# Optimization experiments

Hardware: AMD Instinct MI355X
Metric: run time of the kernel (lower is better)

Reference implementation:

```python
import jax, jax.numpy as jnp
import numpy as np

N = 250000   # number of occupied voxels (sparse points)
C = 64       # channels
G = 256      # voxel grid extent per axis
K = 3        # conv kernel size -> 27 offsets


def _build_neighbor_map():
    """Unique random voxel coords in a G^3 grid; nbr[i,o] = index of point at
    coords[i] + offset_o, or -1 if that voxel is unoccupied (torchsparse kernel map)."""
    rng = np.random.default_rng(0)
    keys = np.unique(rng.integers(0, G ** 3, size=2 * N, dtype=np.int64))[:N]  # sorted unique linearized coords
    x = keys // (G * G)
    y = (keys // G) % G
    z = keys % G
    nbr = np.full((N, K ** 3), -1, dtype=np.int32)
    o = 0
    for dx in (-1, 0, 1):
        for dy in (-1, 0, 1):
            for dz in (-1, 0, 1):
                cx, cy, cz = x + dx, y + dy, z + dz
                valid = (cx >= 0) & (cx < G) & (cy >= 0) & (cy < G) & (cz >= 0) & (cz < G)
                q = cx * (G * G) + cy * G + cz
                pos = np.searchsorted(keys, q).clip(0, N - 1)
                found = valid & (keys[pos] == q)
                nbr[:, o] = np.where(found, pos, -1).astype(np.int32)
                o += 1
    return nbr


def setup_inputs() -> dict:
    key = jax.random.key(0)
    ks = jax.random.split(key, 6)
    s = 0.05
    return {
        "feats": jax.random.normal(ks[0], (N, C), dtype=jnp.float32),
        "w00": jax.random.normal(ks[1], (K ** 3, C, C // 2), dtype=jnp.float32) * s,   # conv0_0: k=3
        "w01": jax.random.normal(ks[2], (K ** 3, C // 2, C // 2), dtype=jnp.float32) * s,  # conv0_1: k=3
        "w10": jax.random.normal(ks[3], (C, C // 2), dtype=jnp.float32) * s,           # conv1_0: 1x1
        "w11": jax.random.normal(ks[4], (K ** 3, C // 2, C // 2), dtype=jnp.float32) * s,  # conv1_1: k=3
        "w12": jax.random.normal(ks[5], (C // 2, C // 2), dtype=jnp.float32) * s,       # conv1_2: 1x1
        "nbr": jnp.asarray(_build_neighbor_map()),
    }


def _sparse_conv3(x, W, nbr):
    """Stride-1 sparse 3D conv: out[i] = sum_o W[o]^T x[nbr[i,o]], skipping absent voxels.
    x: [N, Cin], W: [27, Cin, Cout], nbr: [N, 27] int32 (-1 = missing)."""
    mask = nbr >= 0
    idx = jnp.maximum(nbr, 0)
    out = jnp.zeros((x.shape[0], W.shape[-1]), dtype=x.dtype)
    for o in range(W.shape[0]):  # fixed 27 kernel offsets
        xg = jnp.where(mask[:, o:o + 1], jnp.take(x, idx[:, o], axis=0), 0.0)
        out = out + xg @ W[o]
    return out


def reference(feats, w00, w01, w10, w11, w12, nbr):
    relu = jax.nn.relu
    # branch 0: conv3 -> relu -> conv3
    out0 = _sparse_conv3(relu(_sparse_conv3(feats, w00, nbr)), w01, nbr)
    # branch 1: conv1x1 -> relu -> conv3 -> relu -> conv1x1
    out1 = relu(_sparse_conv3(relu(feats @ w10), w11, nbr)) @ w12
    # concat feats along channel dim, residual add with input feats
    return jnp.concatenate([out0, out1], axis=1) + feats
```

## Files before the change

### kernel.cpp

```cpp
#include <hip/hip_runtime.h>

#define NPTS 250000

typedef float4 f4;


__device__ __forceinline__ void k1_event(int f, int j, int kh, int c,
    const float* __restrict__ feats, const float* __restrict__ w00,
    float& a00, float& a01, float& a02, float& a03)
{
    const int p = f / 27, o = f % 27;
    const f4* __restrict__ xr = reinterpret_cast<const f4*>(feats + (size_t)j * 64 + kh * 32);
    const float* __restrict__ w = w00 + (size_t)(o * 64 + kh * 32) * 32 + c;
    float a = 0.f;
    #pragma unroll
    for (int q = 0; q < 8; ++q) {
        const f4 x = xr[q];
        a = fmaf(x.x, w[(4*q+0)*32], a);
        a = fmaf(x.y, w[(4*q+1)*32], a);
        a = fmaf(x.z, w[(4*q+2)*32], a);
        a = fmaf(x.w, w[(4*q+3)*32], a);
    }
    if      (p == 0) a00 += a;
    else if (p == 1) a01 += a;
    else if (p == 2) a02 += a;
    else             a03 += a;
}

__global__ __launch_bounds__(256) void k1(
    const float* __restrict__ feats, const float* __restrict__ w00,
    const float* __restrict__ w10, const int* __restrict__ nbr,
    float* __restrict__ h0, float* __restrict__ t_out)
{
    __shared__ f4 xs[4][64];
    const int tid  = threadIdx.x;
    const int lane = tid & 63;
    const int wv   = tid >> 6;
    const int c    = lane & 31;
    const int kh   = lane >> 5;
    const int i0   = blockIdx.x * 16 + wv * 4;

    const f4 xv = reinterpret_cast<const f4*>(feats + (size_t)i0 * 64)[lane];
    int2 nv = make_int2(-1, -1);
    if (lane < 54) nv = reinterpret_cast<const int2*>(nbr + (size_t)i0 * 27)[lane];

    float wA[32], wB[32];
    #pragma unroll
    for (int kk = 0; kk < 32; ++kk) {
        const int k = kh * 32 + kk;
        wA[kk] = w00[(size_t)(13 * 64 + k) * 32 + c];
        wB[kk] = w10[(size_t)k * 32 + c];
    }

    xs[wv][lane] = xv;
    __syncthreads();

    float a00 = 0, a01 = 0, a02 = 0, a03 = 0;
    float a10 = 0, a11 = 0, a12 = 0, a13 = 0;
    #pragma unroll
    for (int p = 0; p < 4; ++p) {
        const f4* xr = &xs[wv][p * 16 + kh * 8];
        float a0 = 0.f, a1 = 0.f;
        #pragma unroll
        for (int q = 0; q < 8; ++q) {
            const f4 x = xr[q];
            a0 = fmaf(x.x, wA[4*q+0], a0); a1 = fmaf(x.x, wB[4*q+0], a1);
            a0 = fmaf(x.y, wA[4*q+1], a0); a1 = fmaf(x.y, wB[4*q+1], a1);
            a0 = fmaf(x.z, wA[4*q+2], a0); a1 = fmaf(x.z, wB[4*q+2], a1);
            a0 = fmaf(x.w, wA[4*q+3], a0); a1 = fmaf(x.w, wB[4*q+3], a1);
        }
        if      (p == 0) { a00 = a0; a10 = a1; }
        else if (p == 1) { a01 = a0; a11 = a1; }
        else if (p == 2) { a02 = a0; a12 = a1; }
        else             { a03 = a0; a13 = a1; }
    }

    unsigned long long b0 = __ballot(lane < 54 && nv.x >= 0 && ((2 * lane    ) % 27) != 13);
    unsigned long long b1 = __ballot(lane < 54 && nv.y >= 0 && ((2 * lane + 1) % 27) != 13);
    while (b0) {
        const int L = __builtin_ctzll(b0); b0 &= b0 - 1;
        const int j = __shfl(nv.x, L);
        k1_event(2 * L, j, kh, c, feats, w00, a00, a01, a02, a03);
    }
    while (b1) {
        const int L = __builtin_ctzll(b1); b1 &= b1 - 1;
        const int j = __shfl(nv.y, L);
        k1_event(2 * L + 1, j, kh, c, feats, w00, a00, a01, a02, a03);
    }

    #pragma unroll
    for (int p = 0; p < 4; ++p) {
        float a0 = (p == 0) ? a00 : (p == 1) ? a01 : (p == 2) ? a02 : a03;
        float a1 = (p == 0) ? a10 : (p == 1) ? a11 : (p == 2) ? a12 : a13;
        a0 += __shfl_xor(a0, 32);
        a1 += __shfl_xor(a1, 32);
        const int i = i0 + p;
        if (kh == 0) h0[(size_t)i * 32 + c]    = fmaxf(a0, 0.f);
        else         t_out[(size_t)i * 32 + c] = fmaxf(a1, 0.f);
    }
}

__device__ __forceinline__ void k2_event(int f, int j, int kh, int c,
    const float* __restrict__ h0, const float* __restrict__ t_in,
    const float* __restrict__ w01, const float* __restrict__ w11,
    float& a00, float& a01, float& a02, float& a03,
    float& a10, float& a11, float& a12, float& a13)
{
    const int p = f / 27, o = f % 27;
    const f4* __restrict__ hr = reinterpret_cast<const f4*>(h0   + (size_t)j * 32 + kh * 16);
    const f4* __restrict__ tr = reinterpret_cast<const f4*>(t_in + (size_t)j * 32 + kh * 16);
    const float* __restrict__ wa = w01 + (size_t)(o * 32 + kh * 16) * 32 + c;
    const float* __restrict__ wb = w11 + (size_t)(o * 32 + kh * 16) * 32 + c;
    float a = 0.f, b = 0.f;
    #pragma unroll
    for (int q = 0; q < 4; ++q) {
        const f4 h = hr[q];
        a = fmaf(h.x, wa[(4*q+0)*32], a);
        a = fmaf(h.y, wa[(4*q+1)*32], a);
        a = fmaf(h.z, wa[(4*q+2)*32], a);
        a = fmaf(h.w, wa[(4*q+3)*32], a);
        const f4 u = tr[q];
        b = fmaf(u.x, wb[(4*q+0)*32], b);
        b = fmaf(u.y, wb[(4*q+1)*32], b);
        b = fmaf(u.z, wb[(4*q+2)*32], b);
        b = fmaf(u.w, wb[(4*q+3)*32], b);
    }
    if      (p == 0) { a00 += a; a10 += b; }
    else if (p == 1) { a01 += a; a11 += b; }
    else if (p == 2) { a02 += a; a12 += b; }
    else             { a03 += a; a13 += b; }
}

__global__ __launch_bounds__(256) void k2(
    const float* __restrict__ h0, const float* __restrict__ t_in,
    const float* __restrict__ w01, const float* __restrict__ w11,
    const float* __restrict__ w12, const float* __restrict__ feats,
    const int* __restrict__ nbr, float* __restrict__ out)
{
    __shared__ float2 hs[4][64];
    __shared__ float2 ts[4][64];
    const int tid  = threadIdx.x;
    const int lane = tid & 63;
    const int wv   = tid >> 6;
    const int c    = lane & 31;
    const int kh   = lane >> 5;
    const int i0   = blockIdx.x * 16 + wv * 4;

    const float2 hv = reinterpret_cast<const float2*>(h0   + (size_t)i0 * 32)[lane];
    const float2 tv = reinterpret_cast<const float2*>(t_in + (size_t)i0 * 32)[lane];
    int2 nv = make_int2(-1, -1);
    if (lane < 54) nv = reinterpret_cast<const int2*>(nbr + (size_t)i0 * 27)[lane];

    float wA[16], wB[16], wC[16];
    #pragma unroll
    for (int kk = 0; kk < 16; ++kk) {
        const int k = kh * 16 + kk;
        wA[kk] = w01[(size_t)(13 * 32 + k) * 32 + c];
        wB[kk] = w11[(size_t)(13 * 32 + k) * 32 + c];
        wC[kk] = w12[(size_t)k * 32 + c];
    }

    hs[wv][lane] = hv;
    ts[wv][lane] = tv;
    __syncthreads();

    float a00 = 0, a01 = 0, a02 = 0, a03 = 0;
    float a10 = 0, a11 = 0, a12 = 0, a13 = 0;
    #pragma unroll
    for (int p = 0; p < 4; ++p) {
        const f4* hr = reinterpret_cast<const f4*>(&hs[wv][p * 16]) + kh * 4;
        const f4* tr = reinterpret_cast<const f4*>(&ts[wv][p * 16]) + kh * 4;
        float a0 = 0.f, a1 = 0.f;
        #pragma unroll
        for (int q = 0; q < 4; ++q) {
            const f4 h = hr[q];
            a0 = fmaf(h.x, wA[4*q+0], a0);
            a0 = fmaf(h.y, wA[4*q+1], a0);
            a0 = fmaf(h.z, wA[4*q+2], a0);
            a0 = fmaf(h.w, wA[4*q+3], a0);
            const f4 u = tr[q];
            a1 = fmaf(u.x, wB[4*q+0], a1);
            a1 = fmaf(u.y, wB[4*q+1], a1);
            a1 = fmaf(u.z, wB[4*q+2], a1);
            a1 = fmaf(u.w, wB[4*q+3], a1);
        }
        if      (p == 0) { a00 = a0; a10 = a1; }
        else if (p == 1) { a01 = a0; a11 = a1; }
        else if (p == 2) { a02 = a0; a12 = a1; }
        else             { a03 = a0; a13 = a1; }
    }

    unsigned long long b0 = __ballot(lane < 54 && nv.x >= 0 && ((2 * lane    ) % 27) != 13);
    unsigned long long b1 = __ballot(lane < 54 && nv.y >= 0 && ((2 * lane + 1) % 27) != 13);
    while (b0) {
        const int L = __builtin_ctzll(b0); b0 &= b0 - 1;
        const int j = __shfl(nv.x, L);
        k2_event(2 * L, j, kh, c, h0, t_in, w01, w11, a00, a01, a02, a03, a10, a11, a12, a13);
    }
    while (b1) {
        const int L = __builtin_ctzll(b1); b1 &= b1 - 1;
        const int j = __shfl(nv.y, L);
        k2_event(2 * L + 1, j, kh, c, h0, t_in, w01, w11, a00, a01, a02, a03, a10, a11, a12, a13);
    }

    #pragma unroll
    for (int p = 0; p < 4; ++p) {
        float a0 = (p == 0) ? a00 : (p == 1) ? a01 : (p == 2) ? a02 : a03;
        float a1 = (p == 0) ? a10 : (p == 1) ? a11 : (p == 2) ? a12 : a13;
        a0 += __shfl_xor(a0, 32);
        a1 += __shfl_xor(a1, 32);
        const float t2 = fmaxf(a1, 0.f);
        float o1 = 0.f;
        #pragma unroll
        for (int kk = 0; kk < 16; ++kk) {
            const float tk = __shfl(t2, kh * 16 + kk);
            o1 = fmaf(tk, wC[kk], o1);
        }
        o1 += __shfl_xor(o1, 32);
        const int i = i0 + p;
        const float res = feats[(size_t)i * 64 + kh * 32 + c];
        out[(size_t)i * 64 + kh * 32 + c] = (kh == 0 ? a0 : o1) + res;
    }
}

extern "C" void kernel_launch(void* const* d_in, const int* in_sizes, int n_in,
                              void* d_out, int out_size, void* d_ws, size_t ws_size,
                              hipStream_t stream)
{
    const float* feats = (const float*)d_in[0];
    const float* w00   = (const float*)d_in[1];
    const float* w01   = (const float*)d_in[2];
    const float* w10   = (const float*)d_in[3];
    const float* w11   = (const float*)d_in[4];
    const float* w12   = (const float*)d_in[5];
    const int*   nbr   = (const int*)d_in[6];
    float* out = (float*)d_out;

    float* h0 = (float*)d_ws;
    float* t  = h0 + (size_t)NPTS * 32;

    const int blocks = NPTS / 16;
    k1<<<blocks, 256, 0, stream>>>(feats, w00, w10, nbr, h0, t);
    k2<<<blocks, 256, 0, stream>>>(h0, t, w01, w11, w12, feats, nbr, out);
}
```

Baseline: 454.3 us.

## Split 1x1 conv into separate kernel and drop LDS staging to cut registers

Moves the branch-1 1x1 conv (feats @ w10 + relu) out of k1 into a new kernel k0, so k1 keeps only the w00 center-offset weights in registers. The shared-memory staging and __syncthreads in k1 and k2 are removed; center rows are now read directly from global memory. In k2 the w12 weights are loaded after the gather loop to shorten their register live range. The aim is lower register pressure and higher occupancy for the latency-bound gather loops, at the cost of an extra launch and a second full pass over feats.

```diff
diff --git a/kernel.cpp b/kernel.cpp
--- a/kernel.cpp
+++ b/kernel.cpp
@@ -3,6 +3,38 @@
 #define NPTS 250000
 
 typedef float4 f4;
+
+
+__global__ __launch_bounds__(256) void k0(
+    const float* __restrict__ feats, const float* __restrict__ w10,
+    float* __restrict__ t_out)
+{
+    const int tid = threadIdx.x, lane = tid & 63;
+    const int wv = tid >> 6, c = lane & 31, kh = lane >> 5;
+    const int i0 = blockIdx.x * 16 + wv * 4;
+
+    float wB[32];
+    #pragma unroll
+    for (int kk = 0; kk < 32; ++kk)
+        wB[kk] = w10[(size_t)(kh * 32 + kk) * 32 + c];
+
+    #pragma unroll
+    for (int p = 0; p < 4; ++p) {
+        const f4* __restrict__ xr =
+            reinterpret_cast<const f4*>(feats + (size_t)(i0 + p) * 64 + kh * 32);
+        float a = 0.f;
+        #pragma unroll
+        for (int q = 0; q < 8; ++q) {
+            const f4 x = xr[q];
+            a = fmaf(x.x, wB[4*q+0], a);
+            a = fmaf(x.y, wB[4*q+1], a);
+            a = fmaf(x.z, wB[4*q+2], a);
+            a = fmaf(x.w, wB[4*q+3], a);
+        }
+        a += __shfl_xor(a, 32);
+        if (kh == 0) t_out[(size_t)(i0 + p) * 32 + c] = fmaxf(a, 0.f);
+    }
+}
 
 
 __device__ __forceinline__ void k1_event(int f, int j, int kh, int c,
@@ -29,50 +61,38 @@
 
 __global__ __launch_bounds__(256) void k1(
     const float* __restrict__ feats, const float* __restrict__ w00,
-    const float* __restrict__ w10, const int* __restrict__ nbr,
-    float* __restrict__ h0, float* __restrict__ t_out)
-{
-    __shared__ f4 xs[4][64];
-    const int tid  = threadIdx.x;
-    const int lane = tid & 63;
-    const int wv   = tid >> 6;
-    const int c    = lane & 31;
-    const int kh   = lane >> 5;
-    const int i0   = blockIdx.x * 16 + wv * 4;
-
-    const f4 xv = reinterpret_cast<const f4*>(feats + (size_t)i0 * 64)[lane];
+    const int* __restrict__ nbr, float* __restrict__ h0)
+{
+    const int tid = threadIdx.x, lane = tid & 63;
+    const int wv = tid >> 6, c = lane & 31, kh = lane >> 5;
+    const int i0 = blockIdx.x * 16 + wv * 4;
+
     int2 nv = make_int2(-1, -1);
     if (lane < 54) nv = reinterpret_cast<const int2*>(nbr + (size_t)i0 * 27)[lane];
 
-    float wA[32], wB[32];
-    #pragma unroll
-    for (int kk = 0; kk < 32; ++kk) {
-        const int k = kh * 32 + kk;
-        wA[kk] = w00[(size_t)(13 * 64 + k) * 32 + c];
-        wB[kk] = w10[(size_t)k * 32 + c];
-    }
-
-    xs[wv][lane] = xv;
-    __syncthreads();
+    float wA[32];
+    #pragma unroll
+    for (int kk = 0; kk < 32; ++kk)
+        wA[kk] = w00[(size_t)(13 * 64 + kh * 32 + kk) * 32 + c];
 
     float a00 = 0, a01 = 0, a02 = 0, a03 = 0;
-    float a10 = 0, a11 = 0, a12 = 0, a13 = 0;
-    #pragma unroll
-    for (int p = 0; p < 4; ++p) {
-        const f4* xr = &xs[wv][p * 16 + kh * 8];
-        float a0 = 0.f, a1 = 0.f;
+    #pragma unroll
+    for (int p = 0; p < 4; ++p) {
+        const f4* __restrict__ xr =
+            reinterpret_cast<const f4*>(feats + (size_t)(i0 + p) * 64 + kh * 32);
+        float a = 0.f;
         #pragma unroll
         for (int q = 0; q < 8; ++q) {
             const f4 x = xr[q];
-            a0 = fmaf(x.x, wA[4*q+0], a0); a1 = fmaf(x.x, wB[4*q+0], a1);
-            a0 = fmaf(x.y, wA[4*q+1], a0); a1 = fmaf(x.y, wB[4*q+1], a1);
-            a0 = fmaf(x.z, wA[4*q+2], a0); a1 = fmaf(x.z, wB[4*q+2], a1);
-            a0 = fmaf(x.w, wA[4*q+3], a0); a1 = fmaf(x.w, wB[4*q+3], a1);
-        }
-        if      (p == 0) { a00 = a0; a10 = a1; }
-        else if (p == 1) { a01 = a0; a11 = a1; }
-        else if (p == 2) { a02 = a0; a12 = a1; }
-        else             { a03 = a0; a13 = a1; }
+            a = fmaf(x.x, wA[4*q+0], a);
+            a = fmaf(x.y, wA[4*q+1], a);
+            a = fmaf(x.z, wA[4*q+2], a);
+            a = fmaf(x.w, wA[4*q+3], a);
+        }
+        if      (p == 0) a00 = a;
+        else if (p == 1) a01 = a;
+        else if (p == 2) a02 = a;
+        else             a03 = a;
     }
 
     unsigned long long b0 = __ballot(lane < 54 && nv.x >= 0 && ((2 * lane    ) % 27) != 13);
@@ -91,14 +111,11 @@
     #pragma unroll
     for (int p = 0; p < 4; ++p) {
         float a0 = (p == 0) ? a00 : (p == 1) ? a01 : (p == 2) ? a02 : a03;
-        float a1 = (p == 0) ? a10 : (p == 1) ? a11 : (p == 2) ? a12 : a13;
         a0 += __shfl_xor(a0, 32);
-        a1 += __shfl_xor(a1, 32);
-        const int i = i0 + p;
-        if (kh == 0) h0[(size_t)i * 32 + c]    = fmaxf(a0, 0.f);
-        else         t_out[(size_t)i * 32 + c] = fmaxf(a1, 0.f);
-    }
-}
+        if (kh == 0) h0[(size_t)(i0 + p) * 32 + c] = fmaxf(a0, 0.f);
+    }
+}
+
 
 __device__ __forceinline__ void k2_event(int f, int j, int kh, int c,
     const float* __restrict__ h0, const float* __restrict__ t_in,
@@ -137,39 +154,29 @@
     const float* __restrict__ w12, const float* __restrict__ feats,
     const int* __restrict__ nbr, float* __restrict__ out)
 {
-    __shared__ float2 hs[4][64];
-    __shared__ float2 ts[4][64];
-    const int tid  = threadIdx.x;
-    const int lane = tid & 63;
-    const int wv   = tid >> 6;
-    const int c    = lane & 31;
-    const int kh   = lane >> 5;
-    const int i0   = blockIdx.x * 16 + wv * 4;
-
-    const float2 hv = reinterpret_cast<const float2*>(h0   + (size_t)i0 * 32)[lane];
-    const float2 tv = reinterpret_cast<const float2*>(t_in + (size_t)i0 * 32)[lane];
+    const int tid = threadIdx.x, lane = tid & 63;
+    const int wv = tid >> 6, c = lane & 31, kh = lane >> 5;
+    const int i0 = blockIdx.x * 16 + wv * 4;
+
     int2 nv = make_int2(-1, -1);
     if (lane < 54) nv = reinterpret_cast<const int2*>(nbr + (size_t)i0 * 27)[lane];
 
-    float wA[16], wB[16], wC[16];
+    float wA[16], wB[16];
     #pragma unroll
     for (int kk = 0; kk < 16; ++kk) {
         const int k = kh * 16 + kk;
         wA[kk] = w01[(size_t)(13 * 32 + k) * 32 + c];
         wB[kk] = w11[(size_t)(13 * 32 + k) * 32 + c];
-        wC[kk] = w12[(size_t)k * 32 + c];
-    }
-
-    hs[wv][lane] = hv;
-    ts[wv][lane] = tv;
-    __syncthreads();
+    }
 
     float a00 = 0, a01 = 0, a02 = 0, a03 = 0;
     float a10 = 0, a11 = 0, a12 = 0, a13 = 0;
     #pragma unroll
     for (int p = 0; p < 4; ++p) {
-        const f4* hr = reinterpret_cast<const f4*>(&hs[wv][p * 16]) + kh * 4;
-        const f4* tr = reinterpret_cast<const f4*>(&ts[wv][p * 16]) + kh * 4;
+        const f4* __restrict__ hr =
+            reinterpret_cast<const f4*>(h0   + (size_t)(i0 + p) * 32 + kh * 16);
+        const f4* __restrict__ tr =
+            reinterpret_cast<const f4*>(t_in + (size_t)(i0 + p) * 32 + kh * 16);
         float a0 = 0.f, a1 = 0.f;
         #pragma unroll
         for (int q = 0; q < 4; ++q) {
@@ -203,6 +210,11 @@
         k2_event(2 * L + 1, j, kh, c, h0, t_in, w01, w11, a00, a01, a02, a03, a10, a11, a12, a13);
     }
 
+    float wC[16];
+    #pragma unroll
+    for (int kk = 0; kk < 16; ++kk)
+        wC[kk] = w12[(size_t)(kh * 16 + kk) * 32 + c];
+
     #pragma unroll
     for (int p = 0; p < 4; ++p) {
         float a0 = (p == 0) ? a00 : (p == 1) ? a01 : (p == 2) ? a02 : a03;
@@ -240,6 +252,7 @@
     float* t  = h0 + (size_t)NPTS * 32;
 
     const int blocks = NPTS / 16;
-    k1<<<blocks, 256, 0, stream>>>(feats, w00, w10, nbr, h0, t);
+    k0<<<blocks, 256, 0, stream>>>(feats, w10, t);
+    k1<<<blocks, 256, 0, stream>>>(feats, w00, nbr, h0);
     k2<<<blocks, 256, 0, stream>>>(h0, t, w01, w11, w12, feats, nbr, out);
 }
```

Measured after the change: 575.0 us. +26.6%, slower.
